# Performance work log

Hardware: AMD Instinct MI355X
Metric: run time of the kernel (lower is better)

Reference implementation:

```python
import jax, jax.numpy as jnp
import numpy as np

N_NODES = 50000
M_ITEMS = 5000
D_FEAT = 64      # graph node feature dim (input_size)
D_HID = 32       # input_size // 2
D_EMB = 64       # embedding_size = output_size
N_EDGES = 1200000
BATCH = 4096


def _sage_conv(h, src, dst, W_l, b_l, W_r, n_nodes):
    # PyG SAGEConv (mean aggr, root_weight=True):
    # out_i = W_l @ mean_{j in N(i)} h_j + b_l + W_r @ h_i
    msg = h[src]                                              # [E, Din]
    agg = jax.ops.segment_sum(msg, dst, num_segments=n_nodes)  # [N, Din]
    deg = jax.ops.segment_sum(jnp.ones((src.shape[0],), h.dtype), dst,
                              num_segments=n_nodes)
    agg = agg / jnp.maximum(deg, 1.0)[:, None]
    return agg @ W_l.T + b_l + h @ W_r.T


def setup_inputs() -> dict:
    key = jax.random.key(0)
    ks = jax.random.split(key, 12)
    x = jax.random.randint(ks[0], (BATCH,), 0, N_NODES)
    node_x = jax.random.normal(ks[1], (N_NODES, D_FEAT), dtype=jnp.float32)
    edge_index = jax.random.randint(ks[2], (2, N_EDGES), 0, N_NODES)
    rating_mat = jax.random.uniform(ks[3], (N_NODES, M_ITEMS), dtype=jnp.float32)
    s = 0.05
    W_enc = jax.random.normal(ks[4], (D_EMB, M_ITEMS), dtype=jnp.float32) * s
    b_enc = jnp.zeros((D_EMB,), jnp.float32)
    W_dec = jax.random.normal(ks[5], (M_ITEMS, D_EMB), dtype=jnp.float32) * s
    b_dec = jnp.zeros((M_ITEMS,), jnp.float32)
    Wl1 = jax.random.normal(ks[6], (D_HID, D_FEAT), dtype=jnp.float32) * s
    bl1 = jnp.zeros((D_HID,), jnp.float32)
    Wr1 = jax.random.normal(ks[7], (D_HID, D_FEAT), dtype=jnp.float32) * s
    Wl2 = jax.random.normal(ks[8], (D_EMB, D_HID), dtype=jnp.float32) * s
    bl2 = jnp.zeros((D_EMB,), jnp.float32)
    Wr2 = jax.random.normal(ks[9], (D_EMB, D_HID), dtype=jnp.float32) * s
    return {"x": x, "node_x": node_x, "edge_index": edge_index,
            "rating_mat": rating_mat, "W_enc": W_enc, "b_enc": b_enc,
            "W_dec": W_dec, "b_dec": b_dec, "Wl1": Wl1, "bl1": bl1,
            "Wr1": Wr1, "Wl2": Wl2, "bl2": bl2, "Wr2": Wr2}


def reference(x, node_x, edge_index, rating_mat, W_enc, b_enc, W_dec, b_dec,
              Wl1, bl1, Wr1, Wl2, bl2, Wr2):
    src, dst = edge_index[0], edge_index[1]
    # Graph branch (training path, dropout omitted for determinism)
    h = _sage_conv(node_x, src, dst, Wl1, bl1, Wr1, N_NODES)   # [N, D_HID]
    h = jax.nn.relu(h)
    emb_all = _sage_conv(h, src, dst, Wl2, bl2, Wr2, N_NODES)  # [N, D_EMB]
    emb_graph = emb_all[x]                                      # [B, D_EMB]
    # Autoencoder branch
    items = rating_mat[x]                                       # [B, M]
    emb_ae = items @ W_enc.T + b_enc                            # [B, D_EMB]
    out = jax.nn.sigmoid(emb_graph + emb_ae)                    # method='add'
    out = jax.nn.sigmoid(out @ W_dec.T + b_dec)                 # [B, M]
    return out
```

## Files before the change

kernel.cpp:

```cpp
#include <hip/hip_runtime.h>
#include <math.h>

#define N_NODES 50000
#define M_ITEMS 5000
#define D_FEAT 64
#define D_HID 32
#define D_EMB 64
#define N_EDGES 1200000
#define BATCH 4096
#define CAP 80
#define KCH 10
#define KW  500

__device__ __forceinline__ float sigmoidf_(float z) {
    return 1.0f / (1.0f + __expf(-z));
}

#define FILL_BLOCKS  ((N_EDGES + 255) / 256)
#define XW_BLOCKS    ((N_NODES * D_HID + 255) / 256)
#define TR_BLOCKS    ((D_EMB * M_ITEMS + 255) / 256)

__global__ __launch_bounds__(256)
void k_mega1(const int* __restrict__ src, const int* __restrict__ dst,
             int* __restrict__ cursor, int* __restrict__ slot,
             const float* __restrict__ Wenc, float* __restrict__ WencT,
             const float* __restrict__ node_x, const float* __restrict__ Wl1,
             float* __restrict__ y1) {
    __shared__ float wsT[D_FEAT * D_HID];
    const int bid = blockIdx.x;
    if (bid < FILL_BLOCKS) {
        int e = bid * 256 + threadIdx.x;
        if (e < N_EDGES) {
            int dn = dst[e];
            int pos = atomicAdd(&cursor[dn], 1);
            if (pos < CAP) slot[(size_t)dn * CAP + pos] = src[e];
        }
        return;
    }
    if (bid < FILL_BLOCKS + XW_BLOCKS) {
        for (int j = threadIdx.x; j < D_FEAT * D_HID; j += 256) {
            int c = j >> 6, k = j & 63;
            wsT[k * D_HID + c] = Wl1[j];
        }
        __syncthreads();
        int idx = (bid - FILL_BLOCKS) * 256 + threadIdx.x;
        if (idx >= N_NODES * D_HID) return;
        int r = idx >> 5, c = idx & 31;
        const float* xp = node_x + (size_t)r * D_FEAT;
        float s = 0.f;
#pragma unroll
        for (int k = 0; k < D_FEAT; k += 4) {
            float4 xv = *reinterpret_cast<const float4*>(xp + k);
            s = fmaf(xv.x, wsT[(k + 0) * D_HID + c], s);
            s = fmaf(xv.y, wsT[(k + 1) * D_HID + c], s);
            s = fmaf(xv.z, wsT[(k + 2) * D_HID + c], s);
            s = fmaf(xv.w, wsT[(k + 3) * D_HID + c], s);
        }
        y1[idx] = s;
        return;
    }
    {
        int idx = (bid - FILL_BLOCKS - XW_BLOCKS) * 256 + threadIdx.x;
        if (idx >= D_EMB * M_ITEMS) return;
        int e = idx & 63, m = idx >> 6;
        WencT[idx] = Wenc[(size_t)e * M_ITEMS + m];
    }
}

__device__ __forceinline__ int pick4_32(int s0, int s1, int s2, int s3, int j) {
    int v = (j < 32) ? s0 : (j < 64) ? s1 : (j < 96) ? s2 : s3;
    return __shfl(v, j & 31, 32);
}

__global__ __launch_bounds__(256)
void k_node1(const float* __restrict__ node_x, const float* __restrict__ y1,
             const int* __restrict__ cursor, const int* __restrict__ slot,
             const float* __restrict__ Wr1, const float* __restrict__ bl1,
             float* __restrict__ h) {
    __shared__ float wt[D_FEAT * D_HID];
    for (int j = threadIdx.x; j < D_HID * D_FEAT; j += 256) {
        int c = j >> 6, k = j & 63;
        wt[k * D_HID + c] = Wr1[j];
    }
    __syncthreads();
    const int lane = threadIdx.x & 31;
    const int n = blockIdx.x * 8 + (threadIdx.x >> 5);
    const int dgf = cursor[n];
    const int dg = min(dgf, CAP);
    const int* sl = slot + (size_t)n * CAP;
    int s0 = (lane < dg) ? sl[lane] : 0;
    int s1 = (32 + lane < dg) ? sl[32 + lane] : 0;
    int s2 = (64 + lane < dg) ? sl[64 + lane] : 0;
    int s3 = 0;
    float g0 = 0.f, g1 = 0.f, g2 = 0.f, g3 = 0.f;
    int j = 0;
    for (; j + 4 <= dg; j += 4) {
        int a = pick4_32(s0, s1, s2, s3, j);
        int b = pick4_32(s0, s1, s2, s3, j + 1);
        int c = pick4_32(s0, s1, s2, s3, j + 2);
        int d = pick4_32(s0, s1, s2, s3, j + 3);
        g0 += y1[(size_t)a * D_HID + lane];
        g1 += y1[(size_t)b * D_HID + lane];
        g2 += y1[(size_t)c * D_HID + lane];
        g3 += y1[(size_t)d * D_HID + lane];
    }
    for (; j < dg; ++j)
        g0 += y1[(size_t)pick4_32(s0, s1, s2, s3, j) * D_HID + lane];
    float g = ((g0 + g1) + (g2 + g3)) / fmaxf((float)dgf, 1.f) + bl1[lane];
    const float* xp = node_x + (size_t)n * D_FEAT;
    float s = 0.f;
#pragma unroll
    for (int k = 0; k < D_FEAT; k += 4) {
        float4 xv = *reinterpret_cast<const float4*>(xp + k);
        s = fmaf(xv.x, wt[(k + 0) * D_HID + lane], s);
        s = fmaf(xv.y, wt[(k + 1) * D_HID + lane], s);
        s = fmaf(xv.z, wt[(k + 2) * D_HID + lane], s);
        s = fmaf(xv.w, wt[(k + 3) * D_HID + lane], s);
    }
    h[(size_t)n * D_HID + lane] = fmaxf(g + s, 0.f);
}

__global__ __launch_bounds__(512)
void k_enc_part(const int* __restrict__ x, const float* __restrict__ rating,
                const float* __restrict__ WencT, float* __restrict__ part) {
    __shared__ float sm[8192];
    __shared__ int ns[16];
    const int tid = threadIdx.x, lane = tid & 63, wv = tid >> 6;
    const int rb = blockIdx.x * 16;
    const int ky = blockIdx.y;
    if (tid < 16) ns[tid] = x[rb + tid];
    __syncthreads();
    int nh[16];
#pragma unroll
    for (int i = 0; i < 16; ++i)
        nh[i] = __builtin_amdgcn_readfirstlane(ns[i]);
    for (int j4 = tid; j4 < 2000; j4 += 512) {
        int row = j4 / 125, c4 = j4 - row * 125;
        float4 v = *reinterpret_cast<const float4*>(
            rating + (size_t)nh[row] * M_ITEMS + ky * KW + c4 * 4);
        *reinterpret_cast<float4*>(&sm[row * KW + c4 * 4]) = v;
    }
    __syncthreads();
    float acc[16];
#pragma unroll
    for (int i = 0; i < 16; ++i) acc[i] = 0.f;
    for (int g = wv; g < 125; g += 8) {
        int ml = g * 4, gm = ky * KW + ml;
        float w0 = WencT[(size_t)(gm + 0) * 64 + lane];
        float w1 = WencT[(size_t)(gm + 1) * 64 + lane];
        float w2 = WencT[(size_t)(gm + 2) * 64 + lane];
        float w3 = WencT[(size_t)(gm + 3) * 64 + lane];
#pragma unroll
        for (int r = 0; r < 16; ++r) {
            float4 rv = *reinterpret_cast<const float4*>(&sm[r * KW + ml]);
            acc[r] = fmaf(rv.x, w0, acc[r]);
            acc[r] = fmaf(rv.y, w1, acc[r]);
            acc[r] = fmaf(rv.z, w2, acc[r]);
            acc[r] = fmaf(rv.w, w3, acc[r]);
        }
    }
    __syncthreads();
#pragma unroll
    for (int r = 0; r < 16; ++r) sm[(wv * 16 + r) * 64 + lane] = acc[r];
    __syncthreads();
#pragma unroll
    for (int half = 0; half < 2; ++half) {
        int r = wv * 2 + half;
        float s = 0.f;
#pragma unroll
        for (int w = 0; w < 8; ++w) s += sm[(w * 16 + r) * 64 + lane];
        part[((size_t)ky * BATCH + rb + r) * 64 + lane] = s;
    }
}

__global__ __launch_bounds__(512)
void k_comb(const int* __restrict__ x, const float* __restrict__ part,
            const float* __restrict__ benc, const int* __restrict__ cursor,
            const int* __restrict__ slot, const float* __restrict__ h,
            const float* __restrict__ Wl2, const float* __restrict__ bl2,
            const float* __restrict__ Wr2, float* __restrict__ emb) {
    __shared__ float wl2t[D_HID * D_EMB];
    __shared__ float wr2t[D_HID * D_EMB];
    __shared__ float aggl[8][D_HID];
    __shared__ float hl[8][D_HID];
    __shared__ int ns[8];
    const int tid = threadIdx.x, lane = tid & 63, wv = tid >> 6;
    const int rb = blockIdx.x * 8;
    if (tid < 8) ns[tid] = x[rb + tid];
    for (int j = tid; j < D_EMB * D_HID; j += 512) {
        int e = j >> 5, k = j & 31;
        wl2t[k * D_EMB + e] = Wl2[j];
        wr2t[k * D_EMB + e] = Wr2[j];
    }
    __syncthreads();
    const int row = rb + wv;
    const int node = __builtin_amdgcn_readfirstlane(ns[wv]);
    float ae = benc[lane];
#pragma unroll
    for (int ky = 0; ky < KCH; ++ky)
        ae += part[((size_t)ky * BATCH + row) * 64 + lane];
    const int k32 = lane & 31, hi = lane >> 5;
    const int dgf = cursor[node];
    const int dg = min(dgf, CAP);
    const int* sl = slot + (size_t)node * CAP;
    float a0 = 0.f, a1 = 0.f, a2 = 0.f, a3 = 0.f;
    int t = 0;
    for (; t + 8 <= dg; t += 8) {
        int e0 = sl[t + 0], e1 = sl[t + 1], e2 = sl[t + 2], e3 = sl[t + 3];
        int e4 = sl[t + 4], e5 = sl[t + 5], e6 = sl[t + 6], e7 = sl[t + 7];
        int n0 = hi ? e1 : e0;
        int n1 = hi ? e3 : e2;
        int n2 = hi ? e5 : e4;
        int n3 = hi ? e7 : e6;
        a0 += h[(size_t)n0 * D_HID + k32];
        a1 += h[(size_t)n1 * D_HID + k32];
        a2 += h[(size_t)n2 * D_HID + k32];
        a3 += h[(size_t)n3 * D_HID + k32];
    }
    for (; t < dg; t += 2) {
        int e0 = sl[t];
        int e1 = (t + 1 < dg) ? sl[t + 1] : e0;
        int nb = hi ? e1 : e0;
        if (t + hi < dg) a0 += h[(size_t)nb * D_HID + k32];
    }
    float g = (a0 + a1) + (a2 + a3);
    g += __shfl(g, lane ^ 32, 64);
    if (lane < 32) {
        aggl[wv][k32] = g / fmaxf((float)dgf, 1.f);
        hl[wv][k32] = h[(size_t)node * D_HID + k32];
    }
    float ge = bl2[lane];
#pragma unroll
    for (int k = 0; k < D_HID; ++k)
        ge = fmaf(aggl[wv][k], wl2t[k * D_EMB + lane], ge);
#pragma unroll
    for (int k = 0; k < D_HID; ++k)
        ge = fmaf(hl[wv][k], wr2t[k * D_EMB + lane], ge);
    emb[(size_t)row * D_EMB + lane] = sigmoidf_(ge + ae);
}

__global__ __launch_bounds__(256)
void k_dec(const float* __restrict__ emb, const float* __restrict__ Wdec,
           const float* __restrict__ bdec, float* __restrict__ out) {
    const int tid = threadIdx.x;
    const int b0 = blockIdx.y * 32;
    const int m = blockIdx.x * 256 + tid;
    if (m >= M_ITEMS) return;
    const float* ep = emb + (size_t)b0 * 64;
    float acc[32];
#pragma unroll
    for (int i = 0; i < 32; ++i) acc[i] = 0.f;
    const float* wp = Wdec + (size_t)m * 64;
#pragma unroll
    for (int k = 0; k < 64; k += 4) {
        float4 w = *reinterpret_cast<const float4*>(&wp[k]);
#pragma unroll
        for (int i = 0; i < 32; ++i) {
            float4 e4 = *reinterpret_cast<const float4*>(ep + i * 64 + k);
            acc[i] = fmaf(w.x, e4.x, acc[i]);
            acc[i] = fmaf(w.y, e4.y, acc[i]);
            acc[i] = fmaf(w.z, e4.z, acc[i]);
            acc[i] = fmaf(w.w, e4.w, acc[i]);
        }
    }
    float bb = bdec[m];
#pragma unroll
    for (int i = 0; i < 32; ++i)
        out[(size_t)(b0 + i) * M_ITEMS + m] = sigmoidf_(acc[i] + bb);
}

extern "C" void kernel_launch(void* const* d_in, const int* in_sizes, int n_in,
                              void* d_out, int out_size, void* d_ws, size_t ws_size,
                              hipStream_t stream) {
    const int*   x      = (const int*)d_in[0];
    const float* node_x = (const float*)d_in[1];
    const int*   ei     = (const int*)d_in[2];
    const float* rating = (const float*)d_in[3];
    const float* Wenc   = (const float*)d_in[4];
    const float* benc   = (const float*)d_in[5];
    const float* Wdec   = (const float*)d_in[6];
    const float* bdec   = (const float*)d_in[7];
    const float* Wl1    = (const float*)d_in[8];
    const float* bl1    = (const float*)d_in[9];
    const float* Wr1    = (const float*)d_in[10];
    const float* Wl2    = (const float*)d_in[11];
    const float* bl2    = (const float*)d_in[12];
    const float* Wr2    = (const float*)d_in[13];
    const int* src = ei;
    const int* dst = ei + N_EDGES;

    char* w = (char*)d_ws;
    int*   cursor = (int*)w;   w += (size_t)N_NODES * 4;
    int*   slot   = (int*)w;   w += (size_t)N_NODES * CAP * 4;
    float* y1     = (float*)w; w += (size_t)N_NODES * D_HID * 4;
    float* h      = (float*)w; w += (size_t)N_NODES * D_HID * 4;
    float* emb    = (float*)w; w += (size_t)BATCH * D_EMB * 4;
    float* WencT  = (float*)w; w += (size_t)M_ITEMS * D_EMB * 4;
    float* part   = (float*)w; w += (size_t)KCH * BATCH * D_EMB * 4;

    hipMemsetAsync(cursor, 0, (size_t)N_NODES * 4, stream);

    k_mega1<<<FILL_BLOCKS + XW_BLOCKS + TR_BLOCKS, 256, 0, stream>>>(
        src, dst, cursor, slot, Wenc, WencT, node_x, Wl1, y1);
    k_node1<<<N_NODES / 8, 256, 0, stream>>>(
        node_x, y1, cursor, slot, Wr1, bl1, h);
    dim3 genc(BATCH / 16, KCH);
    k_enc_part<<<genc, 512, 0, stream>>>(x, rating, WencT, part);
    k_comb<<<BATCH / 8, 512, 0, stream>>>(
        x, part, benc, cursor, slot, h, Wl2, bl2, Wr2, emb);
    dim3 gdec((M_ITEMS + 255) / 256, BATCH / 32);
    k_dec<<<gdec, 256, 0, stream>>>(emb, Wdec, bdec, (float*)d_out);
}
```

Before: 296.5 us.

## Fuse encoder partial and layer-1 node kernels, use 16-bit neighbor slots

Merges the encoder partial GEMM and the layer-1 SAGE node kernel into one launch with block-range dispatch, so the two independent stages can run concurrently. Neighbor indices are stored as 16-bit values (node ids under 65536) and read eight at a time with one vector load, halving slot traffic. The Wenc transpose now goes through a padded shared-memory tile for coalesced accesses, and the first kernel uses 512-thread blocks. The 16-bit slot format only holds while N_NODES stays below 65536. The 16-element vector loads also assume 16-byte alignment, which holds because CAP*2 is a multiple of 16.

```diff
diff --git a/kernel.cpp b/kernel.cpp
--- a/kernel.cpp
+++ b/kernel.cpp
@@ -12,38 +12,41 @@
 #define KCH 10
 #define KW  500
 
+typedef unsigned short u16;
+
 __device__ __forceinline__ float sigmoidf_(float z) {
     return 1.0f / (1.0f + __expf(-z));
 }
 
-#define FILL_BLOCKS  ((N_EDGES + 255) / 256)
-#define XW_BLOCKS    ((N_NODES * D_HID + 255) / 256)
-#define TR_BLOCKS    ((D_EMB * M_ITEMS + 255) / 256)
-
-__global__ __launch_bounds__(256)
+#define FILL_BLOCKS  ((N_EDGES + 511) / 512)
+#define XW_BLOCKS    ((N_NODES * D_HID + 511) / 512)
+#define TR_BLOCKS    40
+
+__global__ __launch_bounds__(512)
 void k_mega1(const int* __restrict__ src, const int* __restrict__ dst,
-             int* __restrict__ cursor, int* __restrict__ slot,
+             int* __restrict__ cursor, u16* __restrict__ slot,
              const float* __restrict__ Wenc, float* __restrict__ WencT,
              const float* __restrict__ node_x, const float* __restrict__ Wl1,
              float* __restrict__ y1) {
-    __shared__ float wsT[D_FEAT * D_HID];
-    const int bid = blockIdx.x;
+    __shared__ float sm[8256];
+    const int bid = blockIdx.x, tid = threadIdx.x;
     if (bid < FILL_BLOCKS) {
-        int e = bid * 256 + threadIdx.x;
+        int e = bid * 512 + tid;
         if (e < N_EDGES) {
             int dn = dst[e];
             int pos = atomicAdd(&cursor[dn], 1);
-            if (pos < CAP) slot[(size_t)dn * CAP + pos] = src[e];
+            if (pos < CAP) slot[(size_t)dn * CAP + pos] = (u16)src[e];
         }
         return;
     }
     if (bid < FILL_BLOCKS + XW_BLOCKS) {
-        for (int j = threadIdx.x; j < D_FEAT * D_HID; j += 256) {
+        float* wsT = sm;
+        for (int j = tid; j < D_FEAT * D_HID; j += 512) {
             int c = j >> 6, k = j & 63;
             wsT[k * D_HID + c] = Wl1[j];
         }
         __syncthreads();
-        int idx = (bid - FILL_BLOCKS) * 256 + threadIdx.x;
+        int idx = (bid - FILL_BLOCKS) * 512 + tid;
         if (idx >= N_NODES * D_HID) return;
         int r = idx >> 5, c = idx & 31;
         const float* xp = node_x + (size_t)r * D_FEAT;
@@ -60,123 +63,149 @@
         return;
     }
     {
-        int idx = (bid - FILL_BLOCKS - XW_BLOCKS) * 256 + threadIdx.x;
-        if (idx >= D_EMB * M_ITEMS) return;
-        int e = idx & 63, m = idx >> 6;
-        WencT[idx] = Wenc[(size_t)e * M_ITEMS + m];
-    }
-}
-
-__device__ __forceinline__ int pick4_32(int s0, int s1, int s2, int s3, int j) {
-    int v = (j < 32) ? s0 : (j < 64) ? s1 : (j < 96) ? s2 : s3;
-    return __shfl(v, j & 31, 32);
-}
-
-__global__ __launch_bounds__(256)
-void k_node1(const float* __restrict__ node_x, const float* __restrict__ y1,
-             const int* __restrict__ cursor, const int* __restrict__ slot,
-             const float* __restrict__ Wr1, const float* __restrict__ bl1,
-             float* __restrict__ h) {
-    __shared__ float wt[D_FEAT * D_HID];
-    for (int j = threadIdx.x; j < D_HID * D_FEAT; j += 256) {
-        int c = j >> 6, k = j & 63;
-        wt[k * D_HID + c] = Wr1[j];
-    }
-    __syncthreads();
-    const int lane = threadIdx.x & 31;
-    const int n = blockIdx.x * 8 + (threadIdx.x >> 5);
-    const int dgf = cursor[n];
-    const int dg = min(dgf, CAP);
-    const int* sl = slot + (size_t)n * CAP;
-    int s0 = (lane < dg) ? sl[lane] : 0;
-    int s1 = (32 + lane < dg) ? sl[32 + lane] : 0;
-    int s2 = (64 + lane < dg) ? sl[64 + lane] : 0;
-    int s3 = 0;
-    float g0 = 0.f, g1 = 0.f, g2 = 0.f, g3 = 0.f;
-    int j = 0;
-    for (; j + 4 <= dg; j += 4) {
-        int a = pick4_32(s0, s1, s2, s3, j);
-        int b = pick4_32(s0, s1, s2, s3, j + 1);
-        int c = pick4_32(s0, s1, s2, s3, j + 2);
-        int d = pick4_32(s0, s1, s2, s3, j + 3);
-        g0 += y1[(size_t)a * D_HID + lane];
-        g1 += y1[(size_t)b * D_HID + lane];
-        g2 += y1[(size_t)c * D_HID + lane];
-        g3 += y1[(size_t)d * D_HID + lane];
-    }
-    for (; j < dg; ++j)
-        g0 += y1[(size_t)pick4_32(s0, s1, s2, s3, j) * D_HID + lane];
-    float g = ((g0 + g1) + (g2 + g3)) / fmaxf((float)dgf, 1.f) + bl1[lane];
-    const float* xp = node_x + (size_t)n * D_FEAT;
-    float s = 0.f;
-#pragma unroll
-    for (int k = 0; k < D_FEAT; k += 4) {
-        float4 xv = *reinterpret_cast<const float4*>(xp + k);
-        s = fmaf(xv.x, wt[(k + 0) * D_HID + lane], s);
-        s = fmaf(xv.y, wt[(k + 1) * D_HID + lane], s);
-        s = fmaf(xv.z, wt[(k + 2) * D_HID + lane], s);
-        s = fmaf(xv.w, wt[(k + 3) * D_HID + lane], s);
-    }
-    h[(size_t)n * D_HID + lane] = fmaxf(g + s, 0.f);
-}
+        float* tileL = sm;
+        int t = bid - FILL_BLOCKS - XW_BLOCKS;
+        int m0 = t * 128;
+        for (int j = tid; j < 8192; j += 512) {
+            int e = j >> 7, c = j & 127;
+            if (m0 + c < M_ITEMS)
+                tileL[e * 129 + c] = Wenc[(size_t)e * M_ITEMS + m0 + c];
+        }
+        __syncthreads();
+        for (int j = tid; j < 8192; j += 512) {
+            int ep = j & 63, mp = j >> 6;
+            if (m0 + mp < M_ITEMS)
+                WencT[(size_t)(m0 + mp) * 64 + ep] = tileL[ep * 129 + mp];
+        }
+    }
+}
+
+#define ENC_BLOCKS (256 * KCH)
+#define N1_BLOCKS  (N_NODES / 16)
 
 __global__ __launch_bounds__(512)
-void k_enc_part(const int* __restrict__ x, const float* __restrict__ rating,
-                const float* __restrict__ WencT, float* __restrict__ part) {
+void k_mid(const int* __restrict__ x, const float* __restrict__ rating,
+           const float* __restrict__ WencT, float* __restrict__ part,
+           const float* __restrict__ node_x, const float* __restrict__ y1,
+           const int* __restrict__ cursor, const u16* __restrict__ slot,
+           const float* __restrict__ Wr1, const float* __restrict__ bl1,
+           float* __restrict__ h) {
     __shared__ float sm[8192];
     __shared__ int ns[16];
-    const int tid = threadIdx.x, lane = tid & 63, wv = tid >> 6;
-    const int rb = blockIdx.x * 16;
-    const int ky = blockIdx.y;
-    if (tid < 16) ns[tid] = x[rb + tid];
-    __syncthreads();
-    int nh[16];
-#pragma unroll
-    for (int i = 0; i < 16; ++i)
-        nh[i] = __builtin_amdgcn_readfirstlane(ns[i]);
-    for (int j4 = tid; j4 < 2000; j4 += 512) {
-        int row = j4 / 125, c4 = j4 - row * 125;
-        float4 v = *reinterpret_cast<const float4*>(
-            rating + (size_t)nh[row] * M_ITEMS + ky * KW + c4 * 4);
-        *reinterpret_cast<float4*>(&sm[row * KW + c4 * 4]) = v;
-    }
-    __syncthreads();
-    float acc[16];
-#pragma unroll
-    for (int i = 0; i < 16; ++i) acc[i] = 0.f;
-    for (int g = wv; g < 125; g += 8) {
-        int ml = g * 4, gm = ky * KW + ml;
-        float w0 = WencT[(size_t)(gm + 0) * 64 + lane];
-        float w1 = WencT[(size_t)(gm + 1) * 64 + lane];
-        float w2 = WencT[(size_t)(gm + 2) * 64 + lane];
-        float w3 = WencT[(size_t)(gm + 3) * 64 + lane];
-#pragma unroll
-        for (int r = 0; r < 16; ++r) {
-            float4 rv = *reinterpret_cast<const float4*>(&sm[r * KW + ml]);
-            acc[r] = fmaf(rv.x, w0, acc[r]);
-            acc[r] = fmaf(rv.y, w1, acc[r]);
-            acc[r] = fmaf(rv.z, w2, acc[r]);
-            acc[r] = fmaf(rv.w, w3, acc[r]);
-        }
-    }
-    __syncthreads();
-#pragma unroll
-    for (int r = 0; r < 16; ++r) sm[(wv * 16 + r) * 64 + lane] = acc[r];
-    __syncthreads();
-#pragma unroll
-    for (int half = 0; half < 2; ++half) {
-        int r = wv * 2 + half;
-        float s = 0.f;
-#pragma unroll
-        for (int w = 0; w < 8; ++w) s += sm[(w * 16 + r) * 64 + lane];
-        part[((size_t)ky * BATCH + rb + r) * 64 + lane] = s;
+    const int bid = blockIdx.x, tid = threadIdx.x;
+    const int lane = tid & 63, wv = tid >> 6;
+
+    if (bid < ENC_BLOCKS) {
+        const int rb = (bid & 255) * 16;
+        const int ky = bid >> 8;
+        if (tid < 16) ns[tid] = x[rb + tid];
+        __syncthreads();
+        int nh[16];
+#pragma unroll
+        for (int i = 0; i < 16; ++i)
+            nh[i] = __builtin_amdgcn_readfirstlane(ns[i]);
+        for (int j4 = tid; j4 < 2000; j4 += 512) {
+            int row = j4 / 125, c4 = j4 - row * 125;
+            float4 v = *reinterpret_cast<const float4*>(
+                rating + (size_t)nh[row] * M_ITEMS + ky * KW + c4 * 4);
+            *reinterpret_cast<float4*>(&sm[row * KW + c4 * 4]) = v;
+        }
+        __syncthreads();
+        float acc[16];
+#pragma unroll
+        for (int i = 0; i < 16; ++i) acc[i] = 0.f;
+        for (int g = wv; g < 125; g += 8) {
+            int ml = g * 4, gm = ky * KW + ml;
+            float w0 = WencT[(size_t)(gm + 0) * 64 + lane];
+            float w1 = WencT[(size_t)(gm + 1) * 64 + lane];
+            float w2 = WencT[(size_t)(gm + 2) * 64 + lane];
+            float w3 = WencT[(size_t)(gm + 3) * 64 + lane];
+#pragma unroll
+            for (int r = 0; r < 16; ++r) {
+                float4 rv = *reinterpret_cast<const float4*>(&sm[r * KW + ml]);
+                acc[r] = fmaf(rv.x, w0, acc[r]);
+                acc[r] = fmaf(rv.y, w1, acc[r]);
+                acc[r] = fmaf(rv.z, w2, acc[r]);
+                acc[r] = fmaf(rv.w, w3, acc[r]);
+            }
+        }
+        __syncthreads();
+#pragma unroll
+        for (int r = 0; r < 16; ++r) sm[(wv * 16 + r) * 64 + lane] = acc[r];
+        __syncthreads();
+#pragma unroll
+        for (int half = 0; half < 2; ++half) {
+            int r = wv * 2 + half;
+            float s = 0.f;
+#pragma unroll
+            for (int w = 0; w < 8; ++w) s += sm[(w * 16 + r) * 64 + lane];
+            part[((size_t)ky * BATCH + rb + r) * 64 + lane] = s;
+        }
+        return;
+    }
+
+    {
+        float* wt = sm;
+        float* xs = sm + 2048;
+        for (int j = tid; j < D_HID * D_FEAT; j += 512) {
+            int c = j >> 6, k = j & 63;
+            wt[k * D_HID + c] = Wr1[j];
+        }
+        __syncthreads();
+        const int k32 = lane & 31, hi = lane >> 5;
+        const int nb0 = (bid - ENC_BLOCKS) * 16 + wv * 2;
+#pragma unroll
+        for (int nn = 0; nn < 2; ++nn) {
+            const int n = __builtin_amdgcn_readfirstlane(nb0 + nn);
+            const int dgf = cursor[n];
+            const int dg = min(dgf, CAP);
+            const u16* sl = slot + (size_t)n * CAP;
+            float a0 = 0.f, a1 = 0.f, a2 = 0.f, a3 = 0.f;
+            int t = 0;
+            for (; t + 8 <= dg; t += 8) {
+                uint4 w = *reinterpret_cast<const uint4*>(sl + t);
+                int e0 = w.x & 0xFFFF, e1 = w.x >> 16;
+                int e2 = w.y & 0xFFFF, e3 = w.y >> 16;
+                int e4 = w.z & 0xFFFF, e5 = w.z >> 16;
+                int e6 = w.w & 0xFFFF, e7 = w.w >> 16;
+                int n0 = hi ? e1 : e0;
+                int n1 = hi ? e3 : e2;
+                int n2 = hi ? e5 : e4;
+                int n3 = hi ? e7 : e6;
+                a0 += y1[(size_t)n0 * D_HID + k32];
+                a1 += y1[(size_t)n1 * D_HID + k32];
+                a2 += y1[(size_t)n2 * D_HID + k32];
+                a3 += y1[(size_t)n3 * D_HID + k32];
+            }
+            for (; t < dg; t += 2) {
+                int e0 = sl[t];
+                int e1 = (t + 1 < dg) ? sl[t + 1] : e0;
+                int nbr = hi ? e1 : e0;
+                if (t + hi < dg) a0 += y1[(size_t)nbr * D_HID + k32];
+            }
+            float g = (a0 + a1) + (a2 + a3);
+            g += __shfl(g, lane ^ 32, 64);
+            xs[wv * 64 + lane] = node_x[(size_t)n * D_FEAT + lane];
+            if (lane < 32) {
+                float s = g / fmaxf((float)dgf, 1.f) + bl1[k32];
+#pragma unroll
+                for (int kg = 0; kg < 16; ++kg) {
+                    float4 xv = *reinterpret_cast<const float4*>(&xs[wv * 64 + kg * 4]);
+                    s = fmaf(xv.x, wt[(4 * kg + 0) * D_HID + k32], s);
+                    s = fmaf(xv.y, wt[(4 * kg + 1) * D_HID + k32], s);
+                    s = fmaf(xv.z, wt[(4 * kg + 2) * D_HID + k32], s);
+                    s = fmaf(xv.w, wt[(4 * kg + 3) * D_HID + k32], s);
+                }
+                h[(size_t)n * D_HID + k32] = fmaxf(s, 0.f);
+            }
+        }
     }
 }
 
 __global__ __launch_bounds__(512)
 void k_comb(const int* __restrict__ x, const float* __restrict__ part,
             const float* __restrict__ benc, const int* __restrict__ cursor,
-            const int* __restrict__ slot, const float* __restrict__ h,
+            const u16* __restrict__ slot, const float* __restrict__ h,
             const float* __restrict__ Wl2, const float* __restrict__ bl2,
             const float* __restrict__ Wr2, float* __restrict__ emb) {
     __shared__ float wl2t[D_HID * D_EMB];
@@ -202,12 +231,15 @@
     const int k32 = lane & 31, hi = lane >> 5;
     const int dgf = cursor[node];
     const int dg = min(dgf, CAP);
-    const int* sl = slot + (size_t)node * CAP;
+    const u16* sl = slot + (size_t)node * CAP;
     float a0 = 0.f, a1 = 0.f, a2 = 0.f, a3 = 0.f;
     int t = 0;
     for (; t + 8 <= dg; t += 8) {
-        int e0 = sl[t + 0], e1 = sl[t + 1], e2 = sl[t + 2], e3 = sl[t + 3];
-        int e4 = sl[t + 4], e5 = sl[t + 5], e6 = sl[t + 6], e7 = sl[t + 7];
+        uint4 w = *reinterpret_cast<const uint4*>(sl + t);
+        int e0 = w.x & 0xFFFF, e1 = w.x >> 16;
+        int e2 = w.y & 0xFFFF, e3 = w.y >> 16;
+        int e4 = w.z & 0xFFFF, e5 = w.z >> 16;
+        int e6 = w.w & 0xFFFF, e7 = w.w >> 16;
         int n0 = hi ? e1 : e0;
         int n1 = hi ? e3 : e2;
         int n2 = hi ? e5 : e4;
@@ -220,8 +252,8 @@
     for (; t < dg; t += 2) {
         int e0 = sl[t];
         int e1 = (t + 1 < dg) ? sl[t + 1] : e0;
-        int nb = hi ? e1 : e0;
-        if (t + hi < dg) a0 += h[(size_t)nb * D_HID + k32];
+        int nbr = hi ? e1 : e0;
+        if (t + hi < dg) a0 += h[(size_t)nbr * D_HID + k32];
     }
     float g = (a0 + a1) + (a2 + a3);
     g += __shfl(g, lane ^ 32, 64);
@@ -291,7 +323,7 @@
 
     char* w = (char*)d_ws;
     int*   cursor = (int*)w;   w += (size_t)N_NODES * 4;
-    int*   slot   = (int*)w;   w += (size_t)N_NODES * CAP * 4;
+    u16*   slot   = (u16*)w;   w += (size_t)N_NODES * CAP * 2;
     float* y1     = (float*)w; w += (size_t)N_NODES * D_HID * 4;
     float* h      = (float*)w; w += (size_t)N_NODES * D_HID * 4;
     float* emb    = (float*)w; w += (size_t)BATCH * D_EMB * 4;
@@ -300,12 +332,10 @@
 
     hipMemsetAsync(cursor, 0, (size_t)N_NODES * 4, stream);
 
-    k_mega1<<<FILL_BLOCKS + XW_BLOCKS + TR_BLOCKS, 256, 0, stream>>>(
+    k_mega1<<<FILL_BLOCKS + XW_BLOCKS + TR_BLOCKS, 512, 0, stream>>>(
         src, dst, cursor, slot, Wenc, WencT, node_x, Wl1, y1);
-    k_node1<<<N_NODES / 8, 256, 0, stream>>>(
-        node_x, y1, cursor, slot, Wr1, bl1, h);
-    dim3 genc(BATCH / 16, KCH);
-    k_enc_part<<<genc, 512, 0, stream>>>(x, rating, WencT, part);
+    k_mid<<<ENC_BLOCKS + N1_BLOCKS, 512, 0, stream>>>(
+        x, rating, WencT, part, node_x, y1, cursor, slot, Wr1, bl1, h);
     k_comb<<<BATCH / 8, 512, 0, stream>>>(
         x, part, benc, cursor, slot, h, Wl2, bl2, Wr2, emb);
     dim3 gdec((M_ITEMS + 255) / 256, BATCH / 32);
```

Measured after the change: 318.9 us. 1.08x slower.

## Store graph intermediates in bf16 and neighbour slots as u16 with wider gathers

Applied to the files above, without the earlier changes.

Stores the layer-1 projected features and hidden activations as bf16 and the neighbour slot table as 16-bit indices, halving gather and slot traffic. Reworks the node and combine gather loops so each 64-lane wave fetches four neighbours per load, with 16 lanes each reading packed bf16 pairs, then reduces across lanes. Adds rounding error from bf16 intermediates, and the u16 indices rely on the node count staying below 65536.

```diff
diff --git a/kernel.cpp b/kernel.cpp
--- a/kernel.cpp
+++ b/kernel.cpp
@@ -12,8 +12,19 @@
 #define KCH 10
 #define KW  500
 
+typedef unsigned short u16;
+typedef unsigned int u32;
+
 __device__ __forceinline__ float sigmoidf_(float z) {
     return 1.0f / (1.0f + __expf(-z));
+}
+__device__ __forceinline__ u16 f2bf(float f) {
+    u32 b = __float_as_uint(f);
+    b += 0x7FFFu + ((b >> 16) & 1u);
+    return (u16)(b >> 16);
+}
+__device__ __forceinline__ float bf2f(u16 u) {
+    return __uint_as_float(((u32)u) << 16);
 }
 
 #define FILL_BLOCKS  ((N_EDGES + 255) / 256)
@@ -22,10 +33,10 @@
 
 __global__ __launch_bounds__(256)
 void k_mega1(const int* __restrict__ src, const int* __restrict__ dst,
-             int* __restrict__ cursor, int* __restrict__ slot,
+             int* __restrict__ cursor, u16* __restrict__ slot,
              const float* __restrict__ Wenc, float* __restrict__ WencT,
              const float* __restrict__ node_x, const float* __restrict__ Wl1,
-             float* __restrict__ y1) {
+             u16* __restrict__ y1bf) {
     __shared__ float wsT[D_FEAT * D_HID];
     const int bid = blockIdx.x;
     if (bid < FILL_BLOCKS) {
@@ -33,7 +44,7 @@
         if (e < N_EDGES) {
             int dn = dst[e];
             int pos = atomicAdd(&cursor[dn], 1);
-            if (pos < CAP) slot[(size_t)dn * CAP + pos] = src[e];
+            if (pos < CAP) slot[(size_t)dn * CAP + pos] = (u16)src[e];
         }
         return;
     }
@@ -56,7 +67,7 @@
             s = fmaf(xv.z, wsT[(k + 2) * D_HID + c], s);
             s = fmaf(xv.w, wsT[(k + 3) * D_HID + c], s);
         }
-        y1[idx] = s;
+        y1bf[idx] = f2bf(s);
         return;
     }
     {
@@ -67,57 +78,66 @@
     }
 }
 
-__device__ __forceinline__ int pick4_32(int s0, int s1, int s2, int s3, int j) {
-    int v = (j < 32) ? s0 : (j < 64) ? s1 : (j < 96) ? s2 : s3;
-    return __shfl(v, j & 31, 32);
-}
-
 __global__ __launch_bounds__(256)
-void k_node1(const float* __restrict__ node_x, const float* __restrict__ y1,
-             const int* __restrict__ cursor, const int* __restrict__ slot,
+void k_node1(const float* __restrict__ node_x, const u16* __restrict__ y1bf,
+             const int* __restrict__ cursor, const u16* __restrict__ slot,
              const float* __restrict__ Wr1, const float* __restrict__ bl1,
-             float* __restrict__ h) {
+             u16* __restrict__ hbf) {
     __shared__ float wt[D_FEAT * D_HID];
+    __shared__ float xs[4][64];
     for (int j = threadIdx.x; j < D_HID * D_FEAT; j += 256) {
         int c = j >> 6, k = j & 63;
         wt[k * D_HID + c] = Wr1[j];
     }
     __syncthreads();
-    const int lane = threadIdx.x & 31;
-    const int n = blockIdx.x * 8 + (threadIdx.x >> 5);
+    const int lane = threadIdx.x & 63;
+    const int wv = threadIdx.x >> 6;
+    const int grp = lane >> 4, f2 = lane & 15;
+    const int n = blockIdx.x * 4 + wv;
     const int dgf = cursor[n];
     const int dg = min(dgf, CAP);
-    const int* sl = slot + (size_t)n * CAP;
-    int s0 = (lane < dg) ? sl[lane] : 0;
-    int s1 = (32 + lane < dg) ? sl[32 + lane] : 0;
-    int s2 = (64 + lane < dg) ? sl[64 + lane] : 0;
-    int s3 = 0;
-    float g0 = 0.f, g1 = 0.f, g2 = 0.f, g3 = 0.f;
-    int j = 0;
-    for (; j + 4 <= dg; j += 4) {
-        int a = pick4_32(s0, s1, s2, s3, j);
-        int b = pick4_32(s0, s1, s2, s3, j + 1);
-        int c = pick4_32(s0, s1, s2, s3, j + 2);
-        int d = pick4_32(s0, s1, s2, s3, j + 3);
-        g0 += y1[(size_t)a * D_HID + lane];
-        g1 += y1[(size_t)b * D_HID + lane];
-        g2 += y1[(size_t)c * D_HID + lane];
-        g3 += y1[(size_t)d * D_HID + lane];
-    }
-    for (; j < dg; ++j)
-        g0 += y1[(size_t)pick4_32(s0, s1, s2, s3, j) * D_HID + lane];
-    float g = ((g0 + g1) + (g2 + g3)) / fmaxf((float)dgf, 1.f) + bl1[lane];
-    const float* xp = node_x + (size_t)n * D_FEAT;
+    const u16* sl = slot + (size_t)n * CAP;
+    int s0 = (lane < dg) ? (int)sl[lane] : 0;
+    int s1 = (64 + lane < dg) ? (int)sl[64 + lane] : 0;
+    const u32* yb = (const u32*)y1bf;
+    float aL0 = 0.f, aH0 = 0.f, aL1 = 0.f, aH1 = 0.f;
+    for (int t = 0; t < dg; t += 8) {
+        int j0 = t + grp, j1 = t + 4 + grp;
+        int w0 = (j0 < 64) ? s0 : s1;
+        int w1 = (j1 < 64) ? s0 : s1;
+        int nb0 = __shfl(w0, j0 & 63, 64);
+        int nb1 = __shfl(w1, j1 & 63, 64);
+        if (j0 < dg) {
+            u32 v = yb[(size_t)nb0 * 16 + f2];
+            aL0 += __uint_as_float(v << 16);
+            aH0 += __uint_as_float(v & 0xFFFF0000u);
+        }
+        if (j1 < dg) {
+            u32 v = yb[(size_t)nb1 * 16 + f2];
+            aL1 += __uint_as_float(v << 16);
+            aH1 += __uint_as_float(v & 0xFFFF0000u);
+        }
+    }
+    float aL = aL0 + aL1, aH = aH0 + aH1;
+    aL += __shfl_xor(aL, 16, 64); aL += __shfl_xor(aL, 32, 64);
+    aH += __shfl_xor(aH, 16, 64); aH += __shfl_xor(aH, 32, 64);
+    const int c = lane & 31, hi = lane >> 5;
+    float vL = __shfl(aL, c >> 1, 64);
+    float vH = __shfl(aH, c >> 1, 64);
+    float aggc = (c & 1) ? vH : vL;
+    xs[wv][lane] = node_x[(size_t)n * D_FEAT + lane];
     float s = 0.f;
 #pragma unroll
-    for (int k = 0; k < D_FEAT; k += 4) {
-        float4 xv = *reinterpret_cast<const float4*>(xp + k);
-        s = fmaf(xv.x, wt[(k + 0) * D_HID + lane], s);
-        s = fmaf(xv.y, wt[(k + 1) * D_HID + lane], s);
-        s = fmaf(xv.z, wt[(k + 2) * D_HID + lane], s);
-        s = fmaf(xv.w, wt[(k + 3) * D_HID + lane], s);
-    }
-    h[(size_t)n * D_HID + lane] = fmaxf(g + s, 0.f);
+    for (int kk = 0; kk < 32; kk += 4) {
+        float4 xv = *reinterpret_cast<const float4*>(&xs[wv][hi * 32 + kk]);
+        s = fmaf(xv.x, wt[(hi * 32 + kk + 0) * D_HID + c], s);
+        s = fmaf(xv.y, wt[(hi * 32 + kk + 1) * D_HID + c], s);
+        s = fmaf(xv.z, wt[(hi * 32 + kk + 2) * D_HID + c], s);
+        s = fmaf(xv.w, wt[(hi * 32 + kk + 3) * D_HID + c], s);
+    }
+    s += __shfl_xor(s, 32, 64);
+    float res = fmaxf(aggc / fmaxf((float)dgf, 1.f) + bl1[c] + s, 0.f);
+    if (lane < 32) hbf[(size_t)n * D_HID + c] = f2bf(res);
 }
 
 __global__ __launch_bounds__(512)
@@ -176,7 +196,7 @@
 __global__ __launch_bounds__(512)
 void k_comb(const int* __restrict__ x, const float* __restrict__ part,
             const float* __restrict__ benc, const int* __restrict__ cursor,
-            const int* __restrict__ slot, const float* __restrict__ h,
+            const u16* __restrict__ slot, const u16* __restrict__ hbf,
             const float* __restrict__ Wl2, const float* __restrict__ bl2,
             const float* __restrict__ Wr2, float* __restrict__ emb) {
     __shared__ float wl2t[D_HID * D_EMB];
@@ -199,35 +219,41 @@
 #pragma unroll
     for (int ky = 0; ky < KCH; ++ky)
         ae += part[((size_t)ky * BATCH + row) * 64 + lane];
-    const int k32 = lane & 31, hi = lane >> 5;
+    const int grp = lane >> 4, f2 = lane & 15;
     const int dgf = cursor[node];
     const int dg = min(dgf, CAP);
-    const int* sl = slot + (size_t)node * CAP;
-    float a0 = 0.f, a1 = 0.f, a2 = 0.f, a3 = 0.f;
-    int t = 0;
-    for (; t + 8 <= dg; t += 8) {
-        int e0 = sl[t + 0], e1 = sl[t + 1], e2 = sl[t + 2], e3 = sl[t + 3];
-        int e4 = sl[t + 4], e5 = sl[t + 5], e6 = sl[t + 6], e7 = sl[t + 7];
-        int n0 = hi ? e1 : e0;
-        int n1 = hi ? e3 : e2;
-        int n2 = hi ? e5 : e4;
-        int n3 = hi ? e7 : e6;
-        a0 += h[(size_t)n0 * D_HID + k32];
-        a1 += h[(size_t)n1 * D_HID + k32];
-        a2 += h[(size_t)n2 * D_HID + k32];
-        a3 += h[(size_t)n3 * D_HID + k32];
-    }
-    for (; t < dg; t += 2) {
-        int e0 = sl[t];
-        int e1 = (t + 1 < dg) ? sl[t + 1] : e0;
-        int nb = hi ? e1 : e0;
-        if (t + hi < dg) a0 += h[(size_t)nb * D_HID + k32];
-    }
-    float g = (a0 + a1) + (a2 + a3);
-    g += __shfl(g, lane ^ 32, 64);
+    const u16* sl = slot + (size_t)node * CAP;
+    int s0 = (lane < dg) ? (int)sl[lane] : 0;
+    int s1 = (64 + lane < dg) ? (int)sl[64 + lane] : 0;
+    const u32* hb = (const u32*)hbf;
+    float aL0 = 0.f, aH0 = 0.f, aL1 = 0.f, aH1 = 0.f;
+    for (int t = 0; t < dg; t += 8) {
+        int j0 = t + grp, j1 = t + 4 + grp;
+        int w0 = (j0 < 64) ? s0 : s1;
+        int w1 = (j1 < 64) ? s0 : s1;
+        int nb0 = __shfl(w0, j0 & 63, 64);
+        int nb1 = __shfl(w1, j1 & 63, 64);
+        if (j0 < dg) {
+            u32 v = hb[(size_t)nb0 * 16 + f2];
+            aL0 += __uint_as_float(v << 16);
+            aH0 += __uint_as_float(v & 0xFFFF0000u);
+        }
+        if (j1 < dg) {
+            u32 v = hb[(size_t)nb1 * 16 + f2];
+            aL1 += __uint_as_float(v << 16);
+            aH1 += __uint_as_float(v & 0xFFFF0000u);
+        }
+    }
+    float aL = aL0 + aL1, aH = aH0 + aH1;
+    aL += __shfl_xor(aL, 16, 64); aL += __shfl_xor(aL, 32, 64);
+    aH += __shfl_xor(aH, 16, 64); aH += __shfl_xor(aH, 32, 64);
+    const int c = lane & 31;
+    float vL = __shfl(aL, c >> 1, 64);
+    float vH = __shfl(aH, c >> 1, 64);
+    float aggc = (c & 1) ? vH : vL;
     if (lane < 32) {
-        aggl[wv][k32] = g / fmaxf((float)dgf, 1.f);
-        hl[wv][k32] = h[(size_t)node * D_HID + k32];
+        aggl[wv][c] = aggc / fmaxf((float)dgf, 1.f);
+        hl[wv][c] = bf2f(hbf[(size_t)node * D_HID + c]);
     }
     float ge = bl2[lane];
 #pragma unroll
@@ -291,9 +317,9 @@
 
     char* w = (char*)d_ws;
     int*   cursor = (int*)w;   w += (size_t)N_NODES * 4;
-    int*   slot   = (int*)w;   w += (size_t)N_NODES * CAP * 4;
-    float* y1     = (float*)w; w += (size_t)N_NODES * D_HID * 4;
-    float* h      = (float*)w; w += (size_t)N_NODES * D_HID * 4;
+    u16*   slot   = (u16*)w;   w += (size_t)N_NODES * CAP * 2;
+    u16*   y1bf   = (u16*)w;   w += (size_t)N_NODES * D_HID * 2;
+    u16*   hbf    = (u16*)w;   w += (size_t)N_NODES * D_HID * 2;
     float* emb    = (float*)w; w += (size_t)BATCH * D_EMB * 4;
     float* WencT  = (float*)w; w += (size_t)M_ITEMS * D_EMB * 4;
     float* part   = (float*)w; w += (size_t)KCH * BATCH * D_EMB * 4;
@@ -301,13 +327,13 @@
     hipMemsetAsync(cursor, 0, (size_t)N_NODES * 4, stream);
 
     k_mega1<<<FILL_BLOCKS + XW_BLOCKS + TR_BLOCKS, 256, 0, stream>>>(
-        src, dst, cursor, slot, Wenc, WencT, node_x, Wl1, y1);
-    k_node1<<<N_NODES / 8, 256, 0, stream>>>(
-        node_x, y1, cursor, slot, Wr1, bl1, h);
+        src, dst, cursor, slot, Wenc, WencT, node_x, Wl1, y1bf);
+    k_node1<<<N_NODES / 4, 256, 0, stream>>>(
+        node_x, y1bf, cursor, slot, Wr1, bl1, hbf);
     dim3 genc(BATCH / 16, KCH);
     k_enc_part<<<genc, 512, 0, stream>>>(x, rating, WencT, part);
     k_comb<<<BATCH / 8, 512, 0, stream>>>(
-        x, part, benc, cursor, slot, h, Wl2, bl2, Wr2, emb);
+        x, part, benc, cursor, slot, hbf, Wl2, bl2, Wr2, emb);
     dim3 gdec((M_ITEMS + 255) / 256, BATCH / 32);
     k_dec<<<gdec, 256, 0, stream>>>(emb, Wdec, bdec, (float*)d_out);
 }
```

Result: slower. 309.9 us (+4.5%).

## Merge node-layer-1 and encoder partial kernels into one interleaved launch

Applied to the files above, without the earlier changes.

Combines the first SAGE node aggregation kernel and the encoder partial-GEMM kernel into a single 512-thread launch, interleaving encoder and node blocks so the compute-heavy and gather-heavy work share the GPU concurrently. Node blocks now cover 16 nodes each and reuse the encoder's shared buffer for the transposed weight. This removes one launch boundary and is meant to let the two independent stages overlap. The risk is that node blocks now run at 512 threads with the larger shared allocation, which may lower occupancy for the gather phase.

```diff
diff --git a/kernel.cpp b/kernel.cpp
--- a/kernel.cpp
+++ b/kernel.cpp
@@ -39,7 +39,7 @@
     }
     if (bid < FILL_BLOCKS + XW_BLOCKS) {
         for (int j = threadIdx.x; j < D_FEAT * D_HID; j += 256) {
-            int c = j >> 6, k = j & 63;
+            int c = j / D_FEAT, k = j % D_FEAT;
             wsT[k * D_HID + c] = Wl1[j];
         }
         __syncthreads();
@@ -67,109 +67,121 @@
     }
 }
 
+#define ENC_BLOCKS 2560
+#define N1_BLOCKS  3125
+#define MID_BLOCKS (ENC_BLOCKS + N1_BLOCKS)
+
 __device__ __forceinline__ int pick4_32(int s0, int s1, int s2, int s3, int j) {
     int v = (j < 32) ? s0 : (j < 64) ? s1 : (j < 96) ? s2 : s3;
     return __shfl(v, j & 31, 32);
 }
 
-__global__ __launch_bounds__(256)
-void k_node1(const float* __restrict__ node_x, const float* __restrict__ y1,
-             const int* __restrict__ cursor, const int* __restrict__ slot,
-             const float* __restrict__ Wr1, const float* __restrict__ bl1,
-             float* __restrict__ h) {
-    __shared__ float wt[D_FEAT * D_HID];
-    for (int j = threadIdx.x; j < D_HID * D_FEAT; j += 256) {
-        int c = j >> 6, k = j & 63;
-        wt[k * D_HID + c] = Wr1[j];
-    }
-    __syncthreads();
-    const int lane = threadIdx.x & 31;
-    const int n = blockIdx.x * 8 + (threadIdx.x >> 5);
-    const int dgf = cursor[n];
-    const int dg = min(dgf, CAP);
-    const int* sl = slot + (size_t)n * CAP;
-    int s0 = (lane < dg) ? sl[lane] : 0;
-    int s1 = (32 + lane < dg) ? sl[32 + lane] : 0;
-    int s2 = (64 + lane < dg) ? sl[64 + lane] : 0;
-    int s3 = 0;
-    float g0 = 0.f, g1 = 0.f, g2 = 0.f, g3 = 0.f;
-    int j = 0;
-    for (; j + 4 <= dg; j += 4) {
-        int a = pick4_32(s0, s1, s2, s3, j);
-        int b = pick4_32(s0, s1, s2, s3, j + 1);
-        int c = pick4_32(s0, s1, s2, s3, j + 2);
-        int d = pick4_32(s0, s1, s2, s3, j + 3);
-        g0 += y1[(size_t)a * D_HID + lane];
-        g1 += y1[(size_t)b * D_HID + lane];
-        g2 += y1[(size_t)c * D_HID + lane];
-        g3 += y1[(size_t)d * D_HID + lane];
-    }
-    for (; j < dg; ++j)
-        g0 += y1[(size_t)pick4_32(s0, s1, s2, s3, j) * D_HID + lane];
-    float g = ((g0 + g1) + (g2 + g3)) / fmaxf((float)dgf, 1.f) + bl1[lane];
-    const float* xp = node_x + (size_t)n * D_FEAT;
-    float s = 0.f;
-#pragma unroll
-    for (int k = 0; k < D_FEAT; k += 4) {
-        float4 xv = *reinterpret_cast<const float4*>(xp + k);
-        s = fmaf(xv.x, wt[(k + 0) * D_HID + lane], s);
-        s = fmaf(xv.y, wt[(k + 1) * D_HID + lane], s);
-        s = fmaf(xv.z, wt[(k + 2) * D_HID + lane], s);
-        s = fmaf(xv.w, wt[(k + 3) * D_HID + lane], s);
-    }
-    h[(size_t)n * D_HID + lane] = fmaxf(g + s, 0.f);
-}
-
 __global__ __launch_bounds__(512)
-void k_enc_part(const int* __restrict__ x, const float* __restrict__ rating,
-                const float* __restrict__ WencT, float* __restrict__ part) {
+void k_mid(const int* __restrict__ x, const float* __restrict__ rating,
+           const float* __restrict__ WencT, float* __restrict__ part,
+           const float* __restrict__ node_x, const float* __restrict__ y1,
+           const int* __restrict__ cursor, const int* __restrict__ slot,
+           const float* __restrict__ Wr1, const float* __restrict__ bl1,
+           float* __restrict__ h) {
     __shared__ float sm[8192];
     __shared__ int ns[16];
-    const int tid = threadIdx.x, lane = tid & 63, wv = tid >> 6;
-    const int rb = blockIdx.x * 16;
-    const int ky = blockIdx.y;
-    if (tid < 16) ns[tid] = x[rb + tid];
-    __syncthreads();
-    int nh[16];
-#pragma unroll
-    for (int i = 0; i < 16; ++i)
-        nh[i] = __builtin_amdgcn_readfirstlane(ns[i]);
-    for (int j4 = tid; j4 < 2000; j4 += 512) {
-        int row = j4 / 125, c4 = j4 - row * 125;
-        float4 v = *reinterpret_cast<const float4*>(
-            rating + (size_t)nh[row] * M_ITEMS + ky * KW + c4 * 4);
-        *reinterpret_cast<float4*>(&sm[row * KW + c4 * 4]) = v;
-    }
-    __syncthreads();
-    float acc[16];
-#pragma unroll
-    for (int i = 0; i < 16; ++i) acc[i] = 0.f;
-    for (int g = wv; g < 125; g += 8) {
-        int ml = g * 4, gm = ky * KW + ml;
-        float w0 = WencT[(size_t)(gm + 0) * 64 + lane];
-        float w1 = WencT[(size_t)(gm + 1) * 64 + lane];
-        float w2 = WencT[(size_t)(gm + 2) * 64 + lane];
-        float w3 = WencT[(size_t)(gm + 3) * 64 + lane];
-#pragma unroll
-        for (int r = 0; r < 16; ++r) {
-            float4 rv = *reinterpret_cast<const float4*>(&sm[r * KW + ml]);
-            acc[r] = fmaf(rv.x, w0, acc[r]);
-            acc[r] = fmaf(rv.y, w1, acc[r]);
-            acc[r] = fmaf(rv.z, w2, acc[r]);
-            acc[r] = fmaf(rv.w, w3, acc[r]);
-        }
-    }
-    __syncthreads();
-#pragma unroll
-    for (int r = 0; r < 16; ++r) sm[(wv * 16 + r) * 64 + lane] = acc[r];
-    __syncthreads();
-#pragma unroll
-    for (int half = 0; half < 2; ++half) {
-        int r = wv * 2 + half;
+    const int bid = blockIdx.x, tid = threadIdx.x;
+    const int lane64 = tid & 63, wv = tid >> 6;
+
+    bool is_enc = (bid < 5120) && ((bid & 1) == 0);
+    if (is_enc) {
+        const int eid = bid >> 1;
+        const int rb = (eid & 255) * 16;
+        const int ky = eid >> 8;
+        if (tid < 16) ns[tid] = x[rb + tid];
+        __syncthreads();
+        int nh[16];
+#pragma unroll
+        for (int i = 0; i < 16; ++i)
+            nh[i] = __builtin_amdgcn_readfirstlane(ns[i]);
+        for (int j4 = tid; j4 < 2000; j4 += 512) {
+            int row = j4 / 125, c4 = j4 - row * 125;
+            float4 v = *reinterpret_cast<const float4*>(
+                rating + (size_t)nh[row] * M_ITEMS + ky * KW + c4 * 4);
+            *reinterpret_cast<float4*>(&sm[row * KW + c4 * 4]) = v;
+        }
+        __syncthreads();
+        float acc[16];
+#pragma unroll
+        for (int i = 0; i < 16; ++i) acc[i] = 0.f;
+        for (int g = wv; g < 125; g += 8) {
+            int ml = g * 4, gm = ky * KW + ml;
+            float w0 = WencT[(size_t)(gm + 0) * 64 + lane64];
+            float w1 = WencT[(size_t)(gm + 1) * 64 + lane64];
+            float w2 = WencT[(size_t)(gm + 2) * 64 + lane64];
+            float w3 = WencT[(size_t)(gm + 3) * 64 + lane64];
+#pragma unroll
+            for (int r = 0; r < 16; ++r) {
+                float4 rv = *reinterpret_cast<const float4*>(&sm[r * KW + ml]);
+                acc[r] = fmaf(rv.x, w0, acc[r]);
+                acc[r] = fmaf(rv.y, w1, acc[r]);
+                acc[r] = fmaf(rv.z, w2, acc[r]);
+                acc[r] = fmaf(rv.w, w3, acc[r]);
+            }
+        }
+        __syncthreads();
+#pragma unroll
+        for (int r = 0; r < 16; ++r) sm[(wv * 16 + r) * 64 + lane64] = acc[r];
+        __syncthreads();
+#pragma unroll
+        for (int half = 0; half < 2; ++half) {
+            int r = wv * 2 + half;
+            float s = 0.f;
+#pragma unroll
+            for (int w = 0; w < 8; ++w) s += sm[(w * 16 + r) * 64 + lane64];
+            part[((size_t)ky * BATCH + rb + r) * 64 + lane64] = s;
+        }
+        return;
+    }
+
+    {
+        const int nid = (bid < 5120) ? (bid >> 1) : (2560 + (bid - 5120));
+        float* wt = sm;
+        for (int j = tid; j < D_HID * D_FEAT; j += 512) {
+            int c = j >> 6, k = j & 63;
+            wt[k * D_HID + c] = Wr1[j];
+        }
+        __syncthreads();
+        const int lane = tid & 31;
+        const int n = nid * 16 + (tid >> 5);
+        const int dgf = cursor[n];
+        const int dg = min(dgf, CAP);
+        const int* sl = slot + (size_t)n * CAP;
+        int s0 = (lane < dg) ? sl[lane] : 0;
+        int s1 = (32 + lane < dg) ? sl[32 + lane] : 0;
+        int s2 = (64 + lane < dg) ? sl[64 + lane] : 0;
+        int s3 = 0;
+        float g0 = 0.f, g1 = 0.f, g2 = 0.f, g3 = 0.f;
+        int j = 0;
+        for (; j + 4 <= dg; j += 4) {
+            int a = pick4_32(s0, s1, s2, s3, j);
+            int b = pick4_32(s0, s1, s2, s3, j + 1);
+            int c = pick4_32(s0, s1, s2, s3, j + 2);
+            int d = pick4_32(s0, s1, s2, s3, j + 3);
+            g0 += y1[(size_t)a * D_HID + lane];
+            g1 += y1[(size_t)b * D_HID + lane];
+            g2 += y1[(size_t)c * D_HID + lane];
+            g3 += y1[(size_t)d * D_HID + lane];
+        }
+        for (; j < dg; ++j)
+            g0 += y1[(size_t)pick4_32(s0, s1, s2, s3, j) * D_HID + lane];
+        float g = ((g0 + g1) + (g2 + g3)) / fmaxf((float)dgf, 1.f) + bl1[lane];
+        const float* xp = node_x + (size_t)n * D_FEAT;
         float s = 0.f;
 #pragma unroll
-        for (int w = 0; w < 8; ++w) s += sm[(w * 16 + r) * 64 + lane];
-        part[((size_t)ky * BATCH + rb + r) * 64 + lane] = s;
+        for (int k = 0; k < D_FEAT; k += 4) {
+            float4 xv = *reinterpret_cast<const float4*>(xp + k);
+            s = fmaf(xv.x, wt[(k + 0) * D_HID + lane], s);
+            s = fmaf(xv.y, wt[(k + 1) * D_HID + lane], s);
+            s = fmaf(xv.z, wt[(k + 2) * D_HID + lane], s);
+            s = fmaf(xv.w, wt[(k + 3) * D_HID + lane], s);
+        }
+        h[(size_t)n * D_HID + lane] = fmaxf(g + s, 0.f);
     }
 }
 
@@ -220,8 +232,8 @@
     for (; t < dg; t += 2) {
         int e0 = sl[t];
         int e1 = (t + 1 < dg) ? sl[t + 1] : e0;
-        int nb = hi ? e1 : e0;
-        if (t + hi < dg) a0 += h[(size_t)nb * D_HID + k32];
+        int nbr = hi ? e1 : e0;
+        if (t + hi < dg) a0 += h[(size_t)nbr * D_HID + k32];
     }
     float g = (a0 + a1) + (a2 + a3);
     g += __shfl(g, lane ^ 32, 64);
@@ -302,10 +314,8 @@
 
     k_mega1<<<FILL_BLOCKS + XW_BLOCKS + TR_BLOCKS, 256, 0, stream>>>(
         src, dst, cursor, slot, Wenc, WencT, node_x, Wl1, y1);
-    k_node1<<<N_NODES / 8, 256, 0, stream>>>(
-        node_x, y1, cursor, slot, Wr1, bl1, h);
-    dim3 genc(BATCH / 16, KCH);
-    k_enc_part<<<genc, 512, 0, stream>>>(x, rating, WencT, part);
+    k_mid<<<MID_BLOCKS, 512, 0, stream>>>(
+        x, rating, WencT, part, node_x, y1, cursor, slot, Wr1, bl1, h);
     k_comb<<<BATCH / 8, 512, 0, stream>>>(
         x, part, benc, cursor, slot, h, Wl2, bl2, Wr2, emb);
     dim3 gdec((M_ITEMS + 255) / 256, BATCH / 32);
```

New measurement: 320.2 us. 8.0% more time.
